# Optimization experiments

Hardware: AMD Instinct MI355X
Metric: run time of the kernel (lower is better)

## Reference

```python
import jax, jax.numpy as jnp
import numpy as np

N_NODES = 100000
N_EDGES = 1600000


def setup_inputs() -> dict:
    key = jax.random.key(0)
    k1, k2, k3, k4 = jax.random.split(key, 4)
    in_c, hid_c, out_c = 128, 128, 64
    x = jax.random.normal(k1, (N_NODES, in_c), dtype=jnp.float32)
    edge_index = jax.random.randint(k2, (2, N_EDGES), 0, N_NODES, dtype=jnp.int64)
    W1 = jax.random.normal(k3, (in_c, hid_c), dtype=jnp.float32) * (1.0 / np.sqrt(in_c))
    b1 = jnp.zeros((hid_c,), dtype=jnp.float32)
    W2 = jax.random.normal(k4, (hid_c, out_c), dtype=jnp.float32) * (1.0 / np.sqrt(hid_c))
    b2 = jnp.zeros((out_c,), dtype=jnp.float32)
    return {"x": x, "edge_index": edge_index, "W1": W1, "b1": b1, "W2": W2, "b2": b2}


def reference(x, edge_index, W1, b1, W2, b2):
    # PyG GCNConv default: add self-loops, symmetric deg normalization, bias.
    N = x.shape[0]
    loops = jnp.arange(N, dtype=edge_index.dtype)
    src = jnp.concatenate([edge_index[0], loops])  # message sources (j)
    dst = jnp.concatenate([edge_index[1], loops])  # aggregation targets (i)
    ones = jnp.ones(src.shape[0], dtype=x.dtype)
    deg = jax.ops.segment_sum(ones, dst, num_segments=N)  # in-degree incl. self-loops
    dis = jnp.where(deg > 0, jax.lax.rsqrt(deg), 0.0)     # deg^{-1/2}, inf->0
    norm = dis[src] * dis[dst]                             # [E+N]

    def gcn(h, W, b):
        h = h @ W                                  # linear transform first (fewer bytes moved)
        msg = h[src] * norm[:, None]               # gather + scale, [E+N, C]
        return jax.ops.segment_sum(msg, dst, num_segments=N) + b

    h = jax.nn.relu(gcn(x, W1, b1))
    return gcn(h, W2, b2)
```

## Files before the change

### kernel.cpp

```cpp
#include <hip/hip_runtime.h>


constexpr int SCAN_CHUNK = 4096;
constexpr int NBKT = 512;
constexpr int EPB  = 8192;
constexpr int CSR_CAP = 12288;

using short8 = __attribute__((ext_vector_type(8))) short;
using f32x4  = __attribute__((ext_vector_type(4))) float;

__device__ __forceinline__ unsigned short f2bf(float f) {
  unsigned u = __float_as_uint(f);
  unsigned r = (u + 0x7FFFu + ((u >> 16) & 1u)) >> 16;
  return (unsigned short)r;
}
__device__ __forceinline__ float bf2f(unsigned short h) {
  return __uint_as_float(((unsigned)h) << 16);
}

__global__ void k_detect(const unsigned* __restrict__ ei, int* __restrict__ flag) {
  if (threadIdx.x == 0 && blockIdx.x == 0) {
    int is64 = 1;
    for (int i = 1; i < 256; i += 2)
      if (ei[i] != 0u) { is64 = 0; break; }
    *flag = is64;
  }
}

__device__ __forceinline__ int ld_idx(const void* ei, int is64, long long i) {
  return is64 ? (int)((const long long*)ei)[i] : ((const int*)ei)[i];
}


__global__ __launch_bounds__(256) void ks_part_g(const int* __restrict__ in,
                                                 int* __restrict__ partial, int m) {
  __shared__ int red[256];
  int b = blockIdx.x, tid = threadIdx.x;
  int base = b * SCAN_CHUNK + tid * 16;
  int s = 0;
#pragma unroll
  for (int i = 0; i < 16; ++i) {
    int idx = base + i;
    if (idx < m) s += in[idx];
  }
  red[tid] = s;
  __syncthreads();
  for (int off = 128; off > 0; off >>= 1) {
    if (tid < off) red[tid] += red[tid + off];
    __syncthreads();
  }
  if (tid == 0) partial[b] = red[0];
}

__global__ __launch_bounds__(256) void k_scan_top(int* __restrict__ partial, int nparts) {
  __shared__ int sums[256];
  int tid = threadIdx.x;
  sums[tid] = (tid < nparts) ? partial[tid] : 0;
  __syncthreads();
  for (int off = 1; off < 256; off <<= 1) {
    int t = (tid >= off) ? sums[tid - off] : 0;
    __syncthreads();
    sums[tid] += t;
    __syncthreads();
  }
  if (tid < nparts) partial[tid] = (tid == 0) ? 0 : sums[tid - 1];
}

__global__ __launch_bounds__(256) void ks_write_g(const int* __restrict__ in,
                                                  const int* __restrict__ partial,
                                                  int* __restrict__ out, int m) {
  __shared__ int tsum[256];
  int b = blockIdx.x, tid = threadIdx.x;
  int base = b * SCAN_CHUNK + tid * 16;
  int vals[16];
  int s = 0;
#pragma unroll
  for (int i = 0; i < 16; ++i) {
    int idx = base + i;
    int v = (idx < m) ? in[idx] : 0;
    vals[i] = s;
    s += v;
  }
  tsum[tid] = s;
  __syncthreads();
  for (int off = 1; off < 256; off <<= 1) {
    int t = (tid >= off) ? tsum[tid - off] : 0;
    __syncthreads();
    tsum[tid] += t;
    __syncthreads();
  }
  int toff = partial[b] + ((tid == 0) ? 0 : tsum[tid - 1]);
#pragma unroll
  for (int i = 0; i < 16; ++i) {
    int idx = base + i;
    if (idx < m) out[idx] = toff + vals[i];
  }
}


__global__ __launch_bounds__(256) void k_hist(const void* __restrict__ ei,
                                              const int* __restrict__ flag,
                                              int* __restrict__ hist,
                                              int e, int nblk, int npb) {
  __shared__ int h[NBKT];
  int blk = blockIdx.x, tid = threadIdx.x;
  for (int i = tid; i < NBKT; i += 256) h[i] = 0;
  __syncthreads();
  int is64 = *flag;
  int base = blk * EPB;
  int end = base + EPB; if (end > e) end = e;
  for (int i = base + tid; i < end; i += 256) {
    int d = ld_idx(ei, is64, (long long)e + i);
    atomicAdd(&h[d / npb], 1);
  }
  __syncthreads();
  for (int i = tid; i < NBKT; i += 256)
    hist[(size_t)i * nblk + blk] = h[i];
}

__global__ __launch_bounds__(256) void k_partition(const void* __restrict__ ei,
                                                   const int* __restrict__ flag,
                                                   const int* __restrict__ scanned,
                                                   unsigned* __restrict__ pairbuf,
                                                   int e, int nblk, int npb) {
  __shared__ int off[NBKT];
  int blk = blockIdx.x, tid = threadIdx.x;
  for (int i = tid; i < NBKT; i += 256)
    off[i] = scanned[(size_t)i * nblk + blk];
  __syncthreads();
  int is64 = *flag;
  int base = blk * EPB;
  int end = base + EPB; if (end > e) end = e;
  for (int i = base + tid; i < end; i += 256) {
    int s = ld_idx(ei, is64, i);
    int d = ld_idx(ei, is64, (long long)e + i);
    int bkt = d / npb;
    int pos = atomicAdd(&off[bkt], 1);
    pairbuf[pos] = (unsigned)s | ((unsigned)(d - bkt * npb) << 20);
  }
}

__global__ __launch_bounds__(256) void k_bucket_all(const unsigned* __restrict__ pairbuf,
                                                    const int* __restrict__ scanned,
                                                    int* __restrict__ rowptr,
                                                    int* __restrict__ cursor,
                                                    float* __restrict__ dis,
                                                    int* __restrict__ csr,
                                                    int n, int e, int npb, int nblk) {
  __shared__ int lcsr[CSR_CAP];
  __shared__ int cnt[256];
  __shared__ int scn[256];
  int b = blockIdx.x, tid = threadIdx.x;
  if (b == 0 && tid == 0) rowptr[n] = e;
  int lo = b * npb;
  if (lo >= n) return;
  int hi = lo + npb; if (hi > n) hi = n;
  int nn = hi - lo;
  int seg_base = scanned[(size_t)b * nblk];
  int seg_end  = (b == NBKT - 1) ? e : scanned[(size_t)(b + 1) * nblk];
  int cnt_total = seg_end - seg_base;

  for (int i = tid; i < nn; i += 256) cnt[i] = 0;
  __syncthreads();
  for (int i = tid; i < cnt_total; i += 256)
    atomicAdd(&cnt[pairbuf[seg_base + i] >> 20], 1);
  __syncthreads();

  int v = (tid < nn) ? cnt[tid] : 0;
  scn[tid] = v;
  __syncthreads();
  for (int off = 1; off < 256; off <<= 1) {
    int t = (tid >= off) ? scn[tid - off] : 0;
    __syncthreads();
    scn[tid] += t;
    __syncthreads();
  }
  int start = (tid == 0) ? 0 : scn[tid - 1];
  if (tid < nn) {
    int node = lo + tid;
    rowptr[node] = seg_base + start;
    cursor[node] = seg_base + start;
    dis[node] = rsqrtf((float)(v + 1));
  }
  __syncthreads();
  if (tid < nn) cnt[tid] = start;
  __syncthreads();

  if (cnt_total <= CSR_CAP) {
    for (int i = tid; i < cnt_total; i += 256) {
      unsigned p = pairbuf[seg_base + i];
      int q = atomicAdd(&cnt[p >> 20], 1);
      lcsr[q] = (int)(p & 0xFFFFFu);
    }
    __syncthreads();
    for (int i = tid; i < cnt_total; i += 256) csr[seg_base + i] = lcsr[i];
  } else {
    for (int i = tid; i < cnt_total; i += 256) {
      unsigned p = pairbuf[seg_base + i];
      int q = atomicAdd(&cursor[lo + (int)(p >> 20)], 1);
      csr[q] = (int)(p & 0xFFFFFu);
    }
  }
}

template <int NCOL, bool XBF16>
__global__ __launch_bounds__(256) void k_gemm_mfma(const void* __restrict__ Xv,
                                                   const float* __restrict__ W,
                                                   const float* __restrict__ dis,
                                                   unsigned short* __restrict__ S,
                                                   int nrows) {
  constexpr int ROWS = 64;
  constexpr int NCF = NCOL / 16;
  __shared__ __align__(16) unsigned short xs[ROWS * 128];
  __shared__ __align__(16) unsigned short wt[NCOL * 128];
  int tid = threadIdx.x;

  for (int id = tid; id < 128 * NCOL; id += 256) {
    int k = id / NCOL, c = id % NCOL;
    wt[(c * 128 + k) ^ ((c & 7) << 3)] = f2bf(W[id]);
  }

  int wv = tid >> 6, lane = tid & 63;
  int l16 = lane & 15, lk = lane >> 4;
  int arow = wv * 16 + l16;
  int npass = (nrows + ROWS - 1) / ROWS;

  for (int p = blockIdx.x; p < npass; p += gridDim.x) {
    int r0 = p * ROWS;
    __syncthreads();
#pragma unroll
    for (int it = 0; it < 4; ++it) {
      int id = tid + 256 * it;
      int row = id >> 4, kc = id & 15;
      int gr = r0 + row;
      unsigned short v[8];
      if (gr < nrows) {
        if (XBF16) {
          const unsigned short* xb = (const unsigned short*)Xv + (size_t)gr * 128 + kc * 8;
#pragma unroll
          for (int j = 0; j < 8; ++j) v[j] = xb[j];
        } else {
          const float4* x4 = (const float4*)Xv + (size_t)gr * 32 + kc * 2;
          float4 f0 = x4[0], f1 = x4[1];
          v[0] = f2bf(f0.x); v[1] = f2bf(f0.y); v[2] = f2bf(f0.z); v[3] = f2bf(f0.w);
          v[4] = f2bf(f1.x); v[5] = f2bf(f1.y); v[6] = f2bf(f1.z); v[7] = f2bf(f1.w);
        }
      } else {
#pragma unroll
        for (int j = 0; j < 8; ++j) v[j] = 0;
      }
      int idx = (row * 128 + kc * 8) ^ ((row & 7) << 3);
      *(short8*)&xs[idx] = *(short8*)v;
    }
    __syncthreads();

    short8 a[4];
#pragma unroll
    for (int ks = 0; ks < 4; ++ks)
      a[ks] = *(short8*)&xs[(arow * 128 + ks * 32 + lk * 8) ^ ((arow & 7) << 3)];

    f32x4 acc[NCF];
#pragma unroll
    for (int cf = 0; cf < NCF; ++cf) acc[cf] = (f32x4){0.f, 0.f, 0.f, 0.f};

#pragma unroll
    for (int cf = 0; cf < NCF; ++cf) {
      int col = cf * 16 + l16;
#pragma unroll
      for (int ks = 0; ks < 4; ++ks) {
        short8 bfr = *(short8*)&wt[(col * 128 + ks * 32 + lk * 8) ^ ((col & 7) << 3)];
        acc[cf] = __builtin_amdgcn_mfma_f32_16x16x32_bf16(a[ks], bfr, acc[cf], 0, 0, 0);
      }
    }

#pragma unroll
    for (int r = 0; r < 4; ++r) {
      int gr = r0 + wv * 16 + lk * 4 + r;
      if (gr < nrows) {
        float dv = dis[gr];
#pragma unroll
        for (int cf = 0; cf < NCF; ++cf)
          S[(size_t)gr * NCOL + cf * 16 + l16] = f2bf(acc[cf][r] * dv);
      }
    }
  }
}

__global__ __launch_bounds__(256) void k_agg1(const unsigned short* __restrict__ S,
                                              const int* __restrict__ rowptr,
                                              const int* __restrict__ csr,
                                              const float* __restrict__ dis,
                                              const float* __restrict__ b,
                                              unsigned short* __restrict__ H, int n) {
  int node = blockIdx.x * 4 + (threadIdx.x >> 6);
  if (node >= n) return;
  int lane = threadIdx.x & 63;
  const ushort2* S2 = (const ushort2*)S;
  ushort2 sv = S2[(size_t)node * 64 + lane];
  float ax = bf2f(sv.x), ay = bf2f(sv.y);
  int lo = rowptr[node], hi = rowptr[node + 1];
  int e = lo;
  for (; e + 3 < hi; e += 4) {
    int j0 = csr[e], j1 = csr[e + 1], j2 = csr[e + 2], j3 = csr[e + 3];
    ushort2 v0 = S2[(size_t)j0 * 64 + lane];
    ushort2 v1 = S2[(size_t)j1 * 64 + lane];
    ushort2 v2 = S2[(size_t)j2 * 64 + lane];
    ushort2 v3 = S2[(size_t)j3 * 64 + lane];
    ax += bf2f(v0.x) + bf2f(v1.x) + bf2f(v2.x) + bf2f(v3.x);
    ay += bf2f(v0.y) + bf2f(v1.y) + bf2f(v2.y) + bf2f(v3.y);
  }
  for (; e < hi; ++e) {
    ushort2 v = S2[(size_t)csr[e] * 64 + lane];
    ax += bf2f(v.x); ay += bf2f(v.y);
  }
  float d = dis[node];
  float2 bb = ((const float2*)b)[lane];
  float hx = fmaxf(fmaf(ax, d, bb.x), 0.f);
  float hy = fmaxf(fmaf(ay, d, bb.y), 0.f);
  ushort2 o; o.x = f2bf(hx); o.y = f2bf(hy);
  ((ushort2*)H)[(size_t)node * 64 + lane] = o;
}

__global__ __launch_bounds__(256) void k_agg2(const unsigned short* __restrict__ S,
                                              const int* __restrict__ rowptr,
                                              const int* __restrict__ csr,
                                              const float* __restrict__ dis,
                                              const float* __restrict__ b,
                                              float* __restrict__ O, int n) {
  int node = blockIdx.x * 4 + (threadIdx.x >> 6);
  if (node >= n) return;
  int lane = threadIdx.x & 63;
  float acc = bf2f(S[(size_t)node * 64 + lane]);
  int lo = rowptr[node], hi = rowptr[node + 1];
  int e = lo;
  for (; e + 3 < hi; e += 4) {
    int j0 = csr[e], j1 = csr[e + 1], j2 = csr[e + 2], j3 = csr[e + 3];
    float v0 = bf2f(S[(size_t)j0 * 64 + lane]);
    float v1 = bf2f(S[(size_t)j1 * 64 + lane]);
    float v2 = bf2f(S[(size_t)j2 * 64 + lane]);
    float v3 = bf2f(S[(size_t)j3 * 64 + lane]);
    acc += v0 + v1 + v2 + v3;
  }
  for (; e < hi; ++e) acc += bf2f(S[(size_t)csr[e] * 64 + lane]);
  O[(size_t)node * 64 + lane] = fmaf(acc, dis[node], b[lane]);
}

extern "C" void kernel_launch(void* const* d_in, const int* in_sizes, int n_in,
                              void* d_out, int out_size, void* d_ws, size_t ws_size,
                              hipStream_t stream) {
  const float* x  = (const float*)d_in[0];
  const void*  ei = d_in[1];
  const float* W1 = (const float*)d_in[2];
  const float* b1 = (const float*)d_in[3];
  const float* W2 = (const float*)d_in[4];
  const float* b2 = (const float*)d_in[5];
  float* out = (float*)d_out;

  const int N = in_sizes[0] / 128;
  const int E = in_sizes[1] / 2;
  const int npb  = (N + NBKT - 1) / NBKT;
  const int nblk = (E + EPB - 1) / EPB;
  const int m    = NBKT * nblk;

  char* w = (char*)d_ws;
  size_t off = 0;
  auto alloc = [&](size_t bytes) -> void* {
    void* p = (void*)(w + off);
    off += (bytes + 255) & ~(size_t)255;
    return p;
  };
  int*            rowptr  = (int*)alloc((size_t)(N + 1) * 4);
  int*            cursor  = (int*)alloc((size_t)N * 4);
  float*          dis     = (float*)alloc((size_t)N * 4);
  int*            csr     = (int*)alloc((size_t)E * 4);
  unsigned*       pairbuf = (unsigned*)alloc((size_t)E * 4);
  int*            hist    = (int*)alloc((size_t)m * 4);
  int*            scanned = (int*)alloc((size_t)m * 4);
  unsigned short* s       = (unsigned short*)alloc((size_t)N * 128 * 2);
  unsigned short* h       = (unsigned short*)alloc((size_t)N * 128 * 2);
  int*            flag    = (int*)alloc(4);
  int*            partial = (int*)alloc(256 * 4);

  int npartsM = (m + SCAN_CHUNK - 1) / SCAN_CHUNK;

  k_detect<<<1, 64, 0, stream>>>((const unsigned*)ei, flag);
  k_hist<<<nblk, 256, 0, stream>>>(ei, flag, hist, E, nblk, npb);
  ks_part_g<<<npartsM, 256, 0, stream>>>(hist, partial, m);
  k_scan_top<<<1, 256, 0, stream>>>(partial, npartsM);
  ks_write_g<<<npartsM, 256, 0, stream>>>(hist, partial, scanned, m);
  k_partition<<<nblk, 256, 0, stream>>>(ei, flag, scanned, pairbuf, E, nblk, npb);
  k_bucket_all<<<NBKT, 256, 0, stream>>>(pairbuf, scanned, rowptr, cursor, dis, csr,
                                         N, E, npb, nblk);

  k_gemm_mfma<128, false><<<1024, 256, 0, stream>>>(x, W1, dis, s, N);
  k_agg1<<<(N + 3) / 4, 256, 0, stream>>>(s, rowptr, csr, dis, b1, h, N);
  k_gemm_mfma<64, true><<<1024, 256, 0, stream>>>(h, W2, dis, s, N);
  k_agg2<<<(N + 3) / 4, 256, 0, stream>>>(s, rowptr, csr, dis, b2, out, N);
}
```

Before: 240.7 us.

## Fuse second-layer linear transform into first aggregation kernel

The W2 GEMM is folded into the layer-1 aggregation kernel. Each block converts W2 to packed bf16 in LDS. After aggregation, each wave stages its node's ReLU output in LDS and computes the 64-wide product with scalar FMAs. This removes the separate MFMA GEMM launch and the write and re-read of the hidden activation buffer. The cost is that all ~25k blocks reload and convert the full W2 matrix. The gather loops are also unrolled from 4 to 8 edges, and the int64 index detection is parallelised across 128 threads.

```diff
diff --git a/kernel.cpp b/kernel.cpp
--- a/kernel.cpp
+++ b/kernel.cpp
@@ -19,12 +19,13 @@
 }
 
 __global__ void k_detect(const unsigned* __restrict__ ei, int* __restrict__ flag) {
-  if (threadIdx.x == 0 && blockIdx.x == 0) {
-    int is64 = 1;
-    for (int i = 1; i < 256; i += 2)
-      if (ei[i] != 0u) { is64 = 0; break; }
-    *flag = is64;
-  }
+  __shared__ int any_nz;
+  int tid = threadIdx.x;
+  if (tid == 0) any_nz = 0;
+  __syncthreads();
+  if (ei[1 + 2 * tid] != 0u) atomicOr(&any_nz, 1);
+  __syncthreads();
+  if (tid == 0) *flag = any_nz ? 0 : 1;
 }
 
 __device__ __forceinline__ int ld_idx(const void* ei, int is64, long long i) {
@@ -286,39 +287,69 @@
   }
 }
 
-__global__ __launch_bounds__(256) void k_agg1(const unsigned short* __restrict__ S,
-                                              const int* __restrict__ rowptr,
-                                              const int* __restrict__ csr,
-                                              const float* __restrict__ dis,
-                                              const float* __restrict__ b,
-                                              unsigned short* __restrict__ H, int n) {
-  int node = blockIdx.x * 4 + (threadIdx.x >> 6);
+__global__ __launch_bounds__(256) void k_agg1_fused(const unsigned short* __restrict__ S,
+                                                    const int* __restrict__ rowptr,
+                                                    const int* __restrict__ csr,
+                                                    const float* __restrict__ dis,
+                                                    const float* __restrict__ b1,
+                                                    const float* __restrict__ W2,
+                                                    unsigned short* __restrict__ S2,
+                                                    int n) {
+  __shared__ unsigned w2l[64 * 64];
+  __shared__ unsigned hsh[4 * 64];
+  int tid = threadIdx.x;
+  for (int i = tid; i < 4096; i += 256) {
+    int k2 = i >> 6, c = i & 63;
+    unsigned loh = f2bf(W2[(2 * k2) * 64 + c]);
+    unsigned hih = f2bf(W2[(2 * k2 + 1) * 64 + c]);
+    w2l[i] = loh | (hih << 16);
+  }
+  __syncthreads();
+
+  int wv = tid >> 6, lane = tid & 63;
+  int node = blockIdx.x * 4 + wv;
   if (node >= n) return;
-  int lane = threadIdx.x & 63;
-  const ushort2* S2 = (const ushort2*)S;
-  ushort2 sv = S2[(size_t)node * 64 + lane];
+
+  const ushort2* S1 = (const ushort2*)S;
+  ushort2 sv = S1[(size_t)node * 64 + lane];
   float ax = bf2f(sv.x), ay = bf2f(sv.y);
   int lo = rowptr[node], hi = rowptr[node + 1];
   int e = lo;
-  for (; e + 3 < hi; e += 4) {
+  for (; e + 7 < hi; e += 8) {
     int j0 = csr[e], j1 = csr[e + 1], j2 = csr[e + 2], j3 = csr[e + 3];
-    ushort2 v0 = S2[(size_t)j0 * 64 + lane];
-    ushort2 v1 = S2[(size_t)j1 * 64 + lane];
-    ushort2 v2 = S2[(size_t)j2 * 64 + lane];
-    ushort2 v3 = S2[(size_t)j3 * 64 + lane];
-    ax += bf2f(v0.x) + bf2f(v1.x) + bf2f(v2.x) + bf2f(v3.x);
-    ay += bf2f(v0.y) + bf2f(v1.y) + bf2f(v2.y) + bf2f(v3.y);
+    int j4 = csr[e + 4], j5 = csr[e + 5], j6 = csr[e + 6], j7 = csr[e + 7];
+    ushort2 v0 = S1[(size_t)j0 * 64 + lane];
+    ushort2 v1 = S1[(size_t)j1 * 64 + lane];
+    ushort2 v2 = S1[(size_t)j2 * 64 + lane];
+    ushort2 v3 = S1[(size_t)j3 * 64 + lane];
+    ushort2 v4 = S1[(size_t)j4 * 64 + lane];
+    ushort2 v5 = S1[(size_t)j5 * 64 + lane];
+    ushort2 v6 = S1[(size_t)j6 * 64 + lane];
+    ushort2 v7 = S1[(size_t)j7 * 64 + lane];
+    ax += (bf2f(v0.x) + bf2f(v1.x)) + (bf2f(v2.x) + bf2f(v3.x)) +
+          (bf2f(v4.x) + bf2f(v5.x)) + (bf2f(v6.x) + bf2f(v7.x));
+    ay += (bf2f(v0.y) + bf2f(v1.y)) + (bf2f(v2.y) + bf2f(v3.y)) +
+          (bf2f(v4.y) + bf2f(v5.y)) + (bf2f(v6.y) + bf2f(v7.y));
   }
   for (; e < hi; ++e) {
-    ushort2 v = S2[(size_t)csr[e] * 64 + lane];
+    ushort2 v = S1[(size_t)csr[e] * 64 + lane];
     ax += bf2f(v.x); ay += bf2f(v.y);
   }
   float d = dis[node];
-  float2 bb = ((const float2*)b)[lane];
+  float2 bb = ((const float2*)b1)[lane];
   float hx = fmaxf(fmaf(ax, d, bb.x), 0.f);
   float hy = fmaxf(fmaf(ay, d, bb.y), 0.f);
-  ushort2 o; o.x = f2bf(hx); o.y = f2bf(hy);
-  ((ushort2*)H)[(size_t)node * 64 + lane] = o;
+  hsh[wv * 64 + lane] = (unsigned)f2bf(hx) | ((unsigned)f2bf(hy) << 16);
+  float acc = 0.f;
+#pragma unroll
+  for (int k2 = 0; k2 < 64; ++k2) {
+    unsigned hp = hsh[wv * 64 + k2];
+    unsigned wp = w2l[k2 * 64 + lane];
+    acc = fmaf(__uint_as_float(hp << 16), __uint_as_float(wp << 16), acc);
+    acc = fmaf(__uint_as_float(hp & 0xFFFF0000u),
+               __uint_as_float(wp & 0xFFFF0000u), acc);
+  }
+  S2[(size_t)node * 64 + lane] = f2bf(acc * d);
 }
 
 __global__ __launch_bounds__(256) void k_agg2(const unsigned short* __restrict__ S,
@@ -333,13 +364,18 @@
   float acc = bf2f(S[(size_t)node * 64 + lane]);
   int lo = rowptr[node], hi = rowptr[node + 1];
   int e = lo;
-  for (; e + 3 < hi; e += 4) {
+  for (; e + 7 < hi; e += 8) {
     int j0 = csr[e], j1 = csr[e + 1], j2 = csr[e + 2], j3 = csr[e + 3];
+    int j4 = csr[e + 4], j5 = csr[e + 5], j6 = csr[e + 6], j7 = csr[e + 7];
     float v0 = bf2f(S[(size_t)j0 * 64 + lane]);
     float v1 = bf2f(S[(size_t)j1 * 64 + lane]);
     float v2 = bf2f(S[(size_t)j2 * 64 + lane]);
     float v3 = bf2f(S[(size_t)j3 * 64 + lane]);
-    acc += v0 + v1 + v2 + v3;
+    float v4 = bf2f(S[(size_t)j4 * 64 + lane]);
+    float v5 = bf2f(S[(size_t)j5 * 64 + lane]);
+    float v6 = bf2f(S[(size_t)j6 * 64 + lane]);
+    float v7 = bf2f(S[(size_t)j7 * 64 + lane]);
+    acc += (v0 + v1) + (v2 + v3) + (v4 + v5) + (v6 + v7);
   }
   for (; e < hi; ++e) acc += bf2f(S[(size_t)csr[e] * 64 + lane]);
   O[(size_t)node * 64 + lane] = fmaf(acc, dis[node], b[lane]);
@@ -376,14 +412,14 @@
   unsigned*       pairbuf = (unsigned*)alloc((size_t)E * 4);
   int*            hist    = (int*)alloc((size_t)m * 4);
   int*            scanned = (int*)alloc((size_t)m * 4);
-  unsigned short* s       = (unsigned short*)alloc((size_t)N * 128 * 2);
-  unsigned short* h       = (unsigned short*)alloc((size_t)N * 128 * 2);
+  unsigned short* s1      = (unsigned short*)alloc((size_t)N * 128 * 2);
+  unsigned short* s2      = (unsigned short*)alloc((size_t)N * 64 * 2);
   int*            flag    = (int*)alloc(4);
   int*            partial = (int*)alloc(256 * 4);
 
   int npartsM = (m + SCAN_CHUNK - 1) / SCAN_CHUNK;
 
-  k_detect<<<1, 64, 0, stream>>>((const unsigned*)ei, flag);
+  k_detect<<<1, 128, 0, stream>>>((const unsigned*)ei, flag);
   k_hist<<<nblk, 256, 0, stream>>>(ei, flag, hist, E, nblk, npb);
   ks_part_g<<<npartsM, 256, 0, stream>>>(hist, partial, m);
   k_scan_top<<<1, 256, 0, stream>>>(partial, npartsM);
@@ -392,8 +428,7 @@
   k_bucket_all<<<NBKT, 256, 0, stream>>>(pairbuf, scanned, rowptr, cursor, dis, csr,
                                          N, E, npb, nblk);
 
-  k_gemm_mfma<128, false><<<1024, 256, 0, stream>>>(x, W1, dis, s, N);
-  k_agg1<<<(N + 3) / 4, 256, 0, stream>>>(s, rowptr, csr, dis, b1, h, N);
-  k_gemm_mfma<64, true><<<1024, 256, 0, stream>>>(h, W2, dis, s, N);
-  k_agg2<<<(N + 3) / 4, 256, 0, stream>>>(s, rowptr, csr, dis, b2, out, N);
-}
+  k_gemm_mfma<128, false><<<1024, 256, 0, stream>>>(x, W1, dis, s1, N);
+  k_agg1_fused<<<(N + 3) / 4, 256, 0, stream>>>(s1, rowptr, csr, dis, b1, W2, s2, N);
+  k_agg2<<<(N + 3) / 4, 256, 0, stream>>>(s2, rowptr, csr, dis, b2, out, N);
+}
```

Measured after the change: 309.0 us. +28.3%, slower.

## Slice feature columns into L2-sized planes for gather aggregation

Applied to the files above, without the earlier changes.

The GEMM now writes its output in a column-sliced layout (8 slices of 16 or 8 bf16 columns, each a contiguous plane over all nodes). The aggregation kernels become persistent grid-stride kernels where each block works on one slice, with lanes split across edges and columns and the partial sums combined by xor-shuffle reductions. The aim is to keep each slice's working set (about 3.2MB or 1.6MB) resident in cache so the random neighbor gathers hit cache instead of HBM. The cost is that each gather fetches only 32 or 16 bytes per node, and the CSR list is re-read once per slice. k_detect is also parallelized across 128 threads.

```diff
diff --git a/kernel.cpp b/kernel.cpp
--- a/kernel.cpp
+++ b/kernel.cpp
@@ -19,12 +19,13 @@
 }
 
 __global__ void k_detect(const unsigned* __restrict__ ei, int* __restrict__ flag) {
-  if (threadIdx.x == 0 && blockIdx.x == 0) {
-    int is64 = 1;
-    for (int i = 1; i < 256; i += 2)
-      if (ei[i] != 0u) { is64 = 0; break; }
-    *flag = is64;
-  }
+  __shared__ int any_nz;
+  int tid = threadIdx.x;
+  if (tid == 0) any_nz = 0;
+  __syncthreads();
+  if (ei[1 + 2 * tid] != 0u) atomicOr(&any_nz, 1);
+  __syncthreads();
+  if (tid == 0) *flag = any_nz ? 0 : 1;
 }
 
 __device__ __forceinline__ int ld_idx(const void* ei, int is64, long long i) {
@@ -203,7 +204,7 @@
   }
 }
 
-template <int NCOL, bool XBF16>
+template <int NCOL, bool XBF16, int SLICE>
 __global__ __launch_bounds__(256) void k_gemm_mfma(const void* __restrict__ Xv,
                                                    const float* __restrict__ W,
                                                    const float* __restrict__ dis,
@@ -279,70 +280,109 @@
       if (gr < nrows) {
         float dv = dis[gr];
 #pragma unroll
-        for (int cf = 0; cf < NCF; ++cf)
-          S[(size_t)gr * NCOL + cf * 16 + l16] = f2bf(acc[cf][r] * dv);
+        for (int cf = 0; cf < NCF; ++cf) {
+          int col = cf * 16 + l16;
+          size_t idx = ((size_t)(col / SLICE) * nrows + gr) * SLICE + (col % SLICE);
+          S[idx] = f2bf(acc[cf][r] * dv);
+        }
       }
     }
   }
 }
 
-__global__ __launch_bounds__(256) void k_agg1(const unsigned short* __restrict__ S,
-                                              const int* __restrict__ rowptr,
-                                              const int* __restrict__ csr,
-                                              const float* __restrict__ dis,
-                                              const float* __restrict__ b,
-                                              unsigned short* __restrict__ H, int n) {
-  int node = blockIdx.x * 4 + (threadIdx.x >> 6);
-  if (node >= n) return;
+__global__ __launch_bounds__(256) void k_agg1_slice(const unsigned short* __restrict__ S1s,
+                                                    const int* __restrict__ rowptr,
+                                                    const int* __restrict__ csr,
+                                                    const float* __restrict__ dis,
+                                                    const float* __restrict__ b1,
+                                                    unsigned short* __restrict__ H,
+                                                    int n, int nwaves) {
+  int slice = blockIdx.x & 7;
+  int wvg = (blockIdx.x >> 3) * 4 + (threadIdx.x >> 6);
   int lane = threadIdx.x & 63;
-  const ushort2* S2 = (const ushort2*)S;
-  ushort2 sv = S2[(size_t)node * 64 + lane];
-  float ax = bf2f(sv.x), ay = bf2f(sv.y);
-  int lo = rowptr[node], hi = rowptr[node + 1];
-  int e = lo;
-  for (; e + 3 < hi; e += 4) {
-    int j0 = csr[e], j1 = csr[e + 1], j2 = csr[e + 2], j3 = csr[e + 3];
-    ushort2 v0 = S2[(size_t)j0 * 64 + lane];
-    ushort2 v1 = S2[(size_t)j1 * 64 + lane];
-    ushort2 v2 = S2[(size_t)j2 * 64 + lane];
-    ushort2 v3 = S2[(size_t)j3 * 64 + lane];
-    ax += bf2f(v0.x) + bf2f(v1.x) + bf2f(v2.x) + bf2f(v3.x);
-    ay += bf2f(v0.y) + bf2f(v1.y) + bf2f(v2.y) + bf2f(v3.y);
-  }
-  for (; e < hi; ++e) {
-    ushort2 v = S2[(size_t)csr[e] * 64 + lane];
-    ax += bf2f(v.x); ay += bf2f(v.y);
-  }
-  float d = dis[node];
-  float2 bb = ((const float2*)b)[lane];
-  float hx = fmaxf(fmaf(ax, d, bb.x), 0.f);
-  float hy = fmaxf(fmaf(ay, d, bb.y), 0.f);
-  ushort2 o; o.x = f2bf(hx); o.y = f2bf(hy);
-  ((ushort2*)H)[(size_t)node * 64 + lane] = o;
-}
-
-__global__ __launch_bounds__(256) void k_agg2(const unsigned short* __restrict__ S,
-                                              const int* __restrict__ rowptr,
-                                              const int* __restrict__ csr,
-                                              const float* __restrict__ dis,
-                                              const float* __restrict__ b,
-                                              float* __restrict__ O, int n) {
-  int node = blockIdx.x * 4 + (threadIdx.x >> 6);
-  if (node >= n) return;
+  int eg = lane >> 3, cp = lane & 7;
+  const unsigned short* base = S1s + (size_t)slice * n * 16;
+  for (int i = wvg; i < n; i += nwaves) {
+    int2 rp = *(const int2*)&rowptr[i];
+    int lo = rp.x, hi = rp.y;
+    float ax = 0.f, ay = 0.f;
+    if (eg == 0) {
+      ushort2 sv = *(const ushort2*)&base[(size_t)i * 16 + cp * 2];
+      ax = bf2f(sv.x); ay = bf2f(sv.y);
+    }
+    int e = lo + eg;
+    for (; e + 8 < hi; e += 16) {
+      int j0 = csr[e], j1 = csr[e + 8];
+      ushort2 v0 = *(const ushort2*)&base[(size_t)j0 * 16 + cp * 2];
+      ushort2 v1 = *(const ushort2*)&base[(size_t)j1 * 16 + cp * 2];
+      ax += bf2f(v0.x) + bf2f(v1.x);
+      ay += bf2f(v0.y) + bf2f(v1.y);
+    }
+    if (e < hi) {
+      int j = csr[e];
+      ushort2 v = *(const ushort2*)&base[(size_t)j * 16 + cp * 2];
+      ax += bf2f(v.x); ay += bf2f(v.y);
+    }
+    ax += __shfl_xor(ax, 8);  ay += __shfl_xor(ay, 8);
+    ax += __shfl_xor(ax, 16); ay += __shfl_xor(ay, 16);
+    ax += __shfl_xor(ax, 32); ay += __shfl_xor(ay, 32);
+    if (eg == 0) {
+      float d = dis[i];
+      float2 bb = ((const float2*)b1)[slice * 8 + cp];
+      ushort2 o;
+      o.x = f2bf(fmaxf(fmaf(ax, d, bb.x), 0.f));
+      o.y = f2bf(fmaxf(fmaf(ay, d, bb.y), 0.f));
+      *(ushort2*)&H[(size_t)i * 128 + slice * 16 + cp * 2] = o;
+    }
+  }
+}
+
+__global__ __launch_bounds__(256) void k_agg2_slice(const unsigned short* __restrict__ S2s,
+                                                    const int* __restrict__ rowptr,
+                                                    const int* __restrict__ csr,
+                                                    const float* __restrict__ dis,
+                                                    const float* __restrict__ b2,
+                                                    float* __restrict__ O,
+                                                    int n, int nwaves) {
+  int slice = blockIdx.x & 7;
+  int wvg = (blockIdx.x >> 3) * 4 + (threadIdx.x >> 6);
   int lane = threadIdx.x & 63;
-  float acc = bf2f(S[(size_t)node * 64 + lane]);
-  int lo = rowptr[node], hi = rowptr[node + 1];
-  int e = lo;
-  for (; e + 3 < hi; e += 4) {
-    int j0 = csr[e], j1 = csr[e + 1], j2 = csr[e + 2], j3 = csr[e + 3];
-    float v0 = bf2f(S[(size_t)j0 * 64 + lane]);
-    float v1 = bf2f(S[(size_t)j1 * 64 + lane]);
-    float v2 = bf2f(S[(size_t)j2 * 64 + lane]);
-    float v3 = bf2f(S[(size_t)j3 * 64 + lane]);
-    acc += v0 + v1 + v2 + v3;
-  }
-  for (; e < hi; ++e) acc += bf2f(S[(size_t)csr[e] * 64 + lane]);
-  O[(size_t)node * 64 + lane] = fmaf(acc, dis[node], b[lane]);
+  int eg = lane >> 2, cp = lane & 3;
+  const unsigned short* base = S2s + (size_t)slice * n * 8;
+  for (int i = wvg; i < n; i += nwaves) {
+    int2 rp = *(const int2*)&rowptr[i];
+    int lo = rp.x, hi = rp.y;
+    float ax = 0.f, ay = 0.f;
+    if (eg == 0) {
+      ushort2 sv = *(const ushort2*)&base[(size_t)i * 8 + cp * 2];
+      ax = bf2f(sv.x); ay = bf2f(sv.y);
+    }
+    int e = lo + eg;
+    for (; e + 16 < hi; e += 32) {
+      int j0 = csr[e], j1 = csr[e + 16];
+      ushort2 v0 = *(const ushort2*)&base[(size_t)j0 * 8 + cp * 2];
+      ushort2 v1 = *(const ushort2*)&base[(size_t)j1 * 8 + cp * 2];
+      ax += bf2f(v0.x) + bf2f(v1.x);
+      ay += bf2f(v0.y) + bf2f(v1.y);
+    }
+    if (e < hi) {
+      int j = csr[e];
+      ushort2 v = *(const ushort2*)&base[(size_t)j * 8 + cp * 2];
+      ax += bf2f(v.x); ay += bf2f(v.y);
+    }
+    ax += __shfl_xor(ax, 4);  ay += __shfl_xor(ay, 4);
+    ax += __shfl_xor(ax, 8);  ay += __shfl_xor(ay, 8);
+    ax += __shfl_xor(ax, 16); ay += __shfl_xor(ay, 16);
+    ax += __shfl_xor(ax, 32); ay += __shfl_xor(ay, 32);
+    if (eg == 0) {
+      float d = dis[i];
+      float2 bb = ((const float2*)b2)[slice * 4 + cp];
+      float2 o;
+      o.x = fmaf(ax, d, bb.x);
+      o.y = fmaf(ay, d, bb.y);
+      *(float2*)&O[(size_t)i * 64 + slice * 8 + cp * 2] = o;
+    }
+  }
 }
 
 extern "C" void kernel_launch(void* const* d_in, const int* in_sizes, int n_in,
@@ -376,14 +416,15 @@
   unsigned*       pairbuf = (unsigned*)alloc((size_t)E * 4);
   int*            hist    = (int*)alloc((size_t)m * 4);
   int*            scanned = (int*)alloc((size_t)m * 4);
-  unsigned short* s       = (unsigned short*)alloc((size_t)N * 128 * 2);
+  unsigned short* s1      = (unsigned short*)alloc((size_t)N * 128 * 2);
+  unsigned short* s2      = (unsigned short*)alloc((size_t)N * 64 * 2);
   unsigned short* h       = (unsigned short*)alloc((size_t)N * 128 * 2);
   int*            flag    = (int*)alloc(4);
   int*            partial = (int*)alloc(256 * 4);
 
   int npartsM = (m + SCAN_CHUNK - 1) / SCAN_CHUNK;
 
-  k_detect<<<1, 64, 0, stream>>>((const unsigned*)ei, flag);
+  k_detect<<<1, 128, 0, stream>>>((const unsigned*)ei, flag);
   k_hist<<<nblk, 256, 0, stream>>>(ei, flag, hist, E, nblk, npb);
   ks_part_g<<<npartsM, 256, 0, stream>>>(hist, partial, m);
   k_scan_top<<<1, 256, 0, stream>>>(partial, npartsM);
@@ -392,8 +433,10 @@
   k_bucket_all<<<NBKT, 256, 0, stream>>>(pairbuf, scanned, rowptr, cursor, dis, csr,
                                          N, E, npb, nblk);
 
-  k_gemm_mfma<128, false><<<1024, 256, 0, stream>>>(x, W1, dis, s, N);
-  k_agg1<<<(N + 3) / 4, 256, 0, stream>>>(s, rowptr, csr, dis, b1, h, N);
-  k_gemm_mfma<64, true><<<1024, 256, 0, stream>>>(h, W2, dis, s, N);
-  k_agg2<<<(N + 3) / 4, 256, 0, stream>>>(s, rowptr, csr, dis, b2, out, N);
-}
+  k_gemm_mfma<128, false, 16><<<1024, 256, 0, stream>>>(x, W1, dis, s1, N);
+  const int AGG_BLOCKS = 2048;
+  const int NW = (AGG_BLOCKS / 8) * 4;
+  k_agg1_slice<<<AGG_BLOCKS, 256, 0, stream>>>(s1, rowptr, csr, dis, b1, h, N, NW);
+  k_gemm_mfma<64, true, 8><<<1024, 256, 0, stream>>>(h, W2, dis, s2, N);
+  k_agg2_slice<<<AGG_BLOCKS, 256, 0, stream>>>(s2, rowptr, csr, dis, b2, out, N, NW);
+}
```

Result: slower. 442.8 us (+83.9%).

## Split aggregation edges across lane groups with 16-byte gathers and shuffle reduce

Applied to the files above, without the earlier changes.

The aggregation kernels now split each wavefront into edge groups (4 groups for 128 columns, 8 for 64) whose lanes load 16-byte bf16 vectors. The groups walk interleaved edges in parallel and are combined with xor shuffles before the epilogue. The goal is more gather loads in flight per node and wider memory transactions, at the cost of the shuffle reduction and idle lanes on low-degree nodes. The degree-detect kernel is parallelised with a shared atomic, and separate S buffers are used for the two layers.

```diff
diff --git a/kernel.cpp b/kernel.cpp
--- a/kernel.cpp
+++ b/kernel.cpp
@@ -19,12 +19,13 @@
 }
 
 __global__ void k_detect(const unsigned* __restrict__ ei, int* __restrict__ flag) {
-  if (threadIdx.x == 0 && blockIdx.x == 0) {
-    int is64 = 1;
-    for (int i = 1; i < 256; i += 2)
-      if (ei[i] != 0u) { is64 = 0; break; }
-    *flag = is64;
-  }
+  __shared__ int any_nz;
+  int tid = threadIdx.x;
+  if (tid == 0) any_nz = 0;
+  __syncthreads();
+  if (ei[1 + 2 * tid] != 0u) atomicOr(&any_nz, 1);
+  __syncthreads();
+  if (tid == 0) *flag = any_nz ? 0 : 1;
 }
 
 __device__ __forceinline__ int ld_idx(const void* ei, int is64, long long i) {
@@ -290,59 +291,111 @@
                                               const int* __restrict__ rowptr,
                                               const int* __restrict__ csr,
                                               const float* __restrict__ dis,
-                                              const float* __restrict__ b,
+                                              const float* __restrict__ b1,
                                               unsigned short* __restrict__ H, int n) {
   int node = blockIdx.x * 4 + (threadIdx.x >> 6);
   if (node >= n) return;
   int lane = threadIdx.x & 63;
-  const ushort2* S2 = (const ushort2*)S;
-  ushort2 sv = S2[(size_t)node * 64 + lane];
-  float ax = bf2f(sv.x), ay = bf2f(sv.y);
-  int lo = rowptr[node], hi = rowptr[node + 1];
-  int e = lo;
-  for (; e + 3 < hi; e += 4) {
-    int j0 = csr[e], j1 = csr[e + 1], j2 = csr[e + 2], j3 = csr[e + 3];
-    ushort2 v0 = S2[(size_t)j0 * 64 + lane];
-    ushort2 v1 = S2[(size_t)j1 * 64 + lane];
-    ushort2 v2 = S2[(size_t)j2 * 64 + lane];
-    ushort2 v3 = S2[(size_t)j3 * 64 + lane];
-    ax += bf2f(v0.x) + bf2f(v1.x) + bf2f(v2.x) + bf2f(v3.x);
-    ay += bf2f(v0.y) + bf2f(v1.y) + bf2f(v2.y) + bf2f(v3.y);
-  }
-  for (; e < hi; ++e) {
-    ushort2 v = S2[(size_t)csr[e] * 64 + lane];
-    ax += bf2f(v.x); ay += bf2f(v.y);
-  }
-  float d = dis[node];
-  float2 bb = ((const float2*)b)[lane];
-  float hx = fmaxf(fmaf(ax, d, bb.x), 0.f);
-  float hy = fmaxf(fmaf(ay, d, bb.y), 0.f);
-  ushort2 o; o.x = f2bf(hx); o.y = f2bf(hy);
-  ((ushort2*)H)[(size_t)node * 64 + lane] = o;
+  int eg = lane >> 4;
+  int cp = lane & 15;
+  float acc[8];
+  if (eg == 0) {
+    short8 v = *(const short8*)&S[(size_t)node * 128 + cp * 8];
+#pragma unroll
+    for (int k = 0; k < 8; ++k) acc[k] = bf2f((unsigned short)v[k]);
+  } else {
+#pragma unroll
+    for (int k = 0; k < 8; ++k) acc[k] = 0.f;
+  }
+  int2 rp = *(const int2*)&rowptr[node];
+  int e = rp.x + eg;
+  for (; e + 4 < rp.y; e += 8) {
+    int j0 = csr[e], j1 = csr[e + 4];
+    short8 v0 = *(const short8*)&S[(size_t)j0 * 128 + cp * 8];
+    short8 v1 = *(const short8*)&S[(size_t)j1 * 128 + cp * 8];
+#pragma unroll
+    for (int k = 0; k < 8; ++k)
+      acc[k] += bf2f((unsigned short)v0[k]) + bf2f((unsigned short)v1[k]);
+  }
+  if (e < rp.y) {
+    int j = csr[e];
+    short8 v = *(const short8*)&S[(size_t)j * 128 + cp * 8];
+#pragma unroll
+    for (int k = 0; k < 8; ++k) acc[k] += bf2f((unsigned short)v[k]);
+  }
+#pragma unroll
+  for (int k = 0; k < 8; ++k) {
+    acc[k] += __shfl_xor(acc[k], 16);
+    acc[k] += __shfl_xor(acc[k], 32);
+  }
+  if (eg == 0) {
+    float d = dis[node];
+    float4 bb0 = ((const float4*)b1)[cp * 2];
+    float4 bb1 = ((const float4*)b1)[cp * 2 + 1];
+    float bv[8] = {bb0.x, bb0.y, bb0.z, bb0.w, bb1.x, bb1.y, bb1.z, bb1.w};
+    short8 o;
+#pragma unroll
+    for (int k = 0; k < 8; ++k)
+      o[k] = (short)f2bf(fmaxf(fmaf(acc[k], d, bv[k]), 0.f));
+    *(short8*)&H[(size_t)node * 128 + cp * 8] = o;
+  }
 }
 
 __global__ __launch_bounds__(256) void k_agg2(const unsigned short* __restrict__ S,
                                               const int* __restrict__ rowptr,
                                               const int* __restrict__ csr,
                                               const float* __restrict__ dis,
-                                              const float* __restrict__ b,
+                                              const float* __restrict__ b2,
                                               float* __restrict__ O, int n) {
   int node = blockIdx.x * 4 + (threadIdx.x >> 6);
   if (node >= n) return;
   int lane = threadIdx.x & 63;
-  float acc = bf2f(S[(size_t)node * 64 + lane]);
-  int lo = rowptr[node], hi = rowptr[node + 1];
-  int e = lo;
-  for (; e + 3 < hi; e += 4) {
-    int j0 = csr[e], j1 = csr[e + 1], j2 = csr[e + 2], j3 = csr[e + 3];
-    float v0 = bf2f(S[(size_t)j0 * 64 + lane]);
-    float v1 = bf2f(S[(size_t)j1 * 64 + lane]);
-    float v2 = bf2f(S[(size_t)j2 * 64 + lane]);
-    float v3 = bf2f(S[(size_t)j3 * 64 + lane]);
-    acc += v0 + v1 + v2 + v3;
-  }
-  for (; e < hi; ++e) acc += bf2f(S[(size_t)csr[e] * 64 + lane]);
-  O[(size_t)node * 64 + lane] = fmaf(acc, dis[node], b[lane]);
+  int eg = lane >> 3;
+  int cp = lane & 7;
+  float acc[8];
+  if (eg == 0) {
+    short8 v = *(const short8*)&S[(size_t)node * 64 + cp * 8];
+#pragma unroll
+    for (int k = 0; k < 8; ++k) acc[k] = bf2f((unsigned short)v[k]);
+  } else {
+#pragma unroll
+    for (int k = 0; k < 8; ++k) acc[k] = 0.f;
+  }
+  int2 rp = *(const int2*)&rowptr[node];
+  int e = rp.x + eg;
+  for (; e + 8 < rp.y; e += 16) {
+    int j0 = csr[e], j1 = csr[e + 8];
+    short8 v0 = *(const short8*)&S[(size_t)j0 * 64 + cp * 8];
+    short8 v1 = *(const short8*)&S[(size_t)j1 * 64 + cp * 8];
+#pragma unroll
+    for (int k = 0; k < 8; ++k)
+      acc[k] += bf2f((unsigned short)v0[k]) + bf2f((unsigned short)v1[k]);
+  }
+  if (e < rp.y) {
+    int j = csr[e];
+    short8 v = *(const short8*)&S[(size_t)j * 64 + cp * 8];
+#pragma unroll
+    for (int k = 0; k < 8; ++k) acc[k] += bf2f((unsigned short)v[k]);
+  }
+#pragma unroll
+  for (int k = 0; k < 8; ++k) {
+    acc[k] += __shfl_xor(acc[k], 8);
+    acc[k] += __shfl_xor(acc[k], 16);
+    acc[k] += __shfl_xor(acc[k], 32);
+  }
+  if (eg == 0) {
+    float d = dis[node];
+    float4 bb0 = ((const float4*)b2)[cp * 2];
+    float4 bb1 = ((const float4*)b2)[cp * 2 + 1];
+    float bv[8] = {bb0.x, bb0.y, bb0.z, bb0.w, bb1.x, bb1.y, bb1.z, bb1.w};
+    float4 o0, o1;
+    o0.x = fmaf(acc[0], d, bv[0]); o0.y = fmaf(acc[1], d, bv[1]);
+    o0.z = fmaf(acc[2], d, bv[2]); o0.w = fmaf(acc[3], d, bv[3]);
+    o1.x = fmaf(acc[4], d, bv[4]); o1.y = fmaf(acc[5], d, bv[5]);
+    o1.z = fmaf(acc[6], d, bv[6]); o1.w = fmaf(acc[7], d, bv[7]);
+    ((float4*)O)[(size_t)node * 16 + cp * 2] = o0;
+    ((float4*)O)[(size_t)node * 16 + cp * 2 + 1] = o1;
+  }
 }
 
 extern "C" void kernel_launch(void* const* d_in, const int* in_sizes, int n_in,
@@ -376,14 +429,15 @@
   unsigned*       pairbuf = (unsigned*)alloc((size_t)E * 4);
   int*            hist    = (int*)alloc((size_t)m * 4);
   int*            scanned = (int*)alloc((size_t)m * 4);
-  unsigned short* s       = (unsigned short*)alloc((size_t)N * 128 * 2);
+  unsigned short* s1      = (unsigned short*)alloc((size_t)N * 128 * 2);
+  unsigned short* s2      = (unsigned short*)alloc((size_t)N * 64 * 2);
   unsigned short* h       = (unsigned short*)alloc((size_t)N * 128 * 2);
   int*            flag    = (int*)alloc(4);
   int*            partial = (int*)alloc(256 * 4);
 
   int npartsM = (m + SCAN_CHUNK - 1) / SCAN_CHUNK;
 
-  k_detect<<<1, 64, 0, stream>>>((const unsigned*)ei, flag);
+  k_detect<<<1, 128, 0, stream>>>((const unsigned*)ei, flag);
   k_hist<<<nblk, 256, 0, stream>>>(ei, flag, hist, E, nblk, npb);
   ks_part_g<<<npartsM, 256, 0, stream>>>(hist, partial, m);
   k_scan_top<<<1, 256, 0, stream>>>(partial, npartsM);
@@ -392,8 +446,8 @@
   k_bucket_all<<<NBKT, 256, 0, stream>>>(pairbuf, scanned, rowptr, cursor, dis, csr,
                                          N, E, npb, nblk);
 
-  k_gemm_mfma<128, false><<<1024, 256, 0, stream>>>(x, W1, dis, s, N);
-  k_agg1<<<(N + 3) / 4, 256, 0, stream>>>(s, rowptr, csr, dis, b1, h, N);
-  k_gemm_mfma<64, true><<<1024, 256, 0, stream>>>(h, W2, dis, s, N);
-  k_agg2<<<(N + 3) / 4, 256, 0, stream>>>(s, rowptr, csr, dis, b2, out, N);
-}
+  k_gemm_mfma<128, false><<<1024, 256, 0, stream>>>(x, W1, dis, s1, N);
+  k_agg1<<<(N + 3) / 4, 256, 0, stream>>>(s1, rowptr, csr, dis, b1, h, N);
+  k_gemm_mfma<64, true><<<1024, 256, 0, stream>>>(h, W2, dis, s2, N);
+  k_agg2<<<(N + 3) / 4, 256, 0, stream>>>(s2, rowptr, csr, dis, b2, out, N);
+}
```

After: 213.1 us. 1.13x faster.
